# Performance work log

Hardware: AMD Instinct MI355X
Metric: run time of the kernel (lower is better)

## Reference

```python
import jax, jax.numpy as jnp
import numpy as np

N = 50000   # nodes
E = 800000  # edges (avg degree 16)
D = 128     # hidden dim (GNN_hidden_dim), heads=1
SLOPE = 0.2  # LeakyReLU negative slope (PyG default)


def _w(k, shape, fan_in):
    return jax.random.normal(k, shape, dtype=jnp.float32) * (1.0 / np.sqrt(fan_in))


def setup_inputs() -> dict:
    key = jax.random.key(0)
    ks = jax.random.split(key, 24)
    inp = {}
    inp["x"] = jax.random.normal(ks[0], (N, D), dtype=jnp.float32)
    inp["edge_index"] = jax.random.randint(ks[1], (2, E), 0, N, dtype=jnp.int32)
    # layer 1 (GATv2 + linear skip)
    inp["Wl1"] = _w(ks[2], (D, D), D); inp["Wr1"] = _w(ks[3], (D, D), D)
    inp["att1"] = _w(ks[4], (D,), D); inp["b1"] = jnp.zeros((D,), jnp.float32)
    inp["Wlin1"] = _w(ks[5], (D, D), D); inp["blin1"] = jnp.zeros((D,), jnp.float32)
    # layer 2
    inp["Wl2"] = _w(ks[6], (D, D), D); inp["Wr2"] = _w(ks[7], (D, D), D)
    inp["att2"] = _w(ks[8], (D,), D); inp["b2"] = jnp.zeros((D,), jnp.float32)
    inp["Wlin2"] = _w(ks[9], (D, D), D); inp["blin2"] = jnp.zeros((D,), jnp.float32)
    # output layer (out_channels=1, heads=1)
    inp["Wlo"] = _w(ks[10], (D, 1), D); inp["Wro"] = _w(ks[11], (D, 1), D)
    inp["atto"] = _w(ks[12], (1,), 1); inp["bo"] = jnp.zeros((1,), jnp.float32)
    inp["Wlino"] = _w(ks[13], (D, 1), D); inp["blino"] = jnp.zeros((1,), jnp.float32)
    return inp


def gatv2(x, src, dst, Wl, Wr, att, b):
    # GATv2 (PyG, add_self_loops=False, share_weights=False, heads=1, no edge_attr)
    xl = x @ Wl            # [N, C] source transform (also message content)
    xr = x @ Wr            # [N, C] target transform
    e = jax.nn.leaky_relu(xl[src] + xr[dst], SLOPE) @ att  # [E] edge logits
    m = jax.ops.segment_max(e, dst, num_segments=N)
    m = jnp.where(jnp.isfinite(m), m, 0.0)  # empty segments
    p = jnp.exp(e - m[dst])
    s = jax.ops.segment_sum(p, dst, num_segments=N)
    alpha = p / (s[dst] + 1e-16)            # segment softmax over incoming edges
    out = jax.ops.segment_sum(alpha[:, None] * xl[src], dst, num_segments=N)
    return out + b


def reference(x, edge_index, Wl1, Wr1, att1, b1, Wlin1, blin1,
              Wl2, Wr2, att2, b2, Wlin2, blin2,
              Wlo, Wro, atto, bo, Wlino, blino):
    src, dst = edge_index[0], edge_index[1]
    h = jax.nn.relu(gatv2(x, src, dst, Wl1, Wr1, att1, b1) + x @ Wlin1 + blin1)
    h = jax.nn.relu(gatv2(h, src, dst, Wl2, Wr2, att2, b2) + h @ Wlin2 + blin2)
    out = gatv2(h, src, dst, Wlo, Wro, atto, bo) + h @ Wlino + blino
    return out  # [N, 1]
```

## Files before the change

### kernel.cpp

```cpp
#include <hip/hip_runtime.h>
#include <hip/hip_fp16.h>
#include <math.h>

#define NN 50000
#define EE 800000
#define DD 128
#define SLOPE 0.2f

typedef __attribute__((ext_vector_type(8))) _Float16 half8;
typedef __attribute__((ext_vector_type(4))) float f32x4;

static __device__ __forceinline__ float wred_sum(float v) {
#pragma unroll
    for (int m = 1; m < 64; m <<= 1) v += __shfl_xor(v, m, 64);
    return v;
}

static __device__ __forceinline__ ushort f2h(float f) {
    __half h = __float2half(f);
    return *reinterpret_cast<ushort*>(&h);
}
static __device__ __forceinline__ __half2 u2h2(unsigned int u) {
    __half2 h;
    *reinterpret_cast<unsigned int*>(&h) = u;
    return h;
}
static __device__ __forceinline__ unsigned int h22u(__half2 h) {
    return *reinterpret_cast<unsigned int*>(&h);
}

__global__ void k_degree(const int* __restrict__ dstv, int* __restrict__ deg,
                         int* __restrict__ epos) {
    int i = blockIdx.x * blockDim.x + threadIdx.x;
    if (i < EE) epos[i] = atomicAdd(&deg[dstv[i]], 1);
}

__global__ void k_blocksum(const int* __restrict__ deg, int* __restrict__ bsum) {
    int t = threadIdx.x;
    int idx = blockIdx.x * 256 + t;
    int v = (idx < NN) ? deg[idx] : 0;
#pragma unroll
    for (int m = 1; m < 64; m <<= 1) v += __shfl_xor(v, m, 64);
    __shared__ int part[4];
    if ((t & 63) == 0) part[t >> 6] = v;
    __syncthreads();
    if (t == 0) bsum[blockIdx.x] = part[0] + part[1] + part[2] + part[3];
}

__global__ void k_scan_bsum(const int* __restrict__ bsum, int* __restrict__ boff, int nb) {
    __shared__ int sd[2][256];
    int t = threadIdx.x;
    int v = (t < nb) ? bsum[t] : 0;
    sd[0][t] = v;
    __syncthreads();
    int s = 0;
    for (int off = 1; off < 256; off <<= 1) {
        int x = sd[s][t];
        if (t >= off) x += sd[s][t - off];
        sd[s ^ 1][t] = x;
        s ^= 1;
        __syncthreads();
    }
    if (t < nb) boff[t] = sd[s][t] - v;
}

__global__ void k_scan_final(const int* __restrict__ deg, const int* __restrict__ boff,
                             int* __restrict__ offs) {
    __shared__ int sd[2][256];
    int t = threadIdx.x;
    int idx = blockIdx.x * 256 + t;
    int v = (idx < NN) ? deg[idx] : 0;
    sd[0][t] = v;
    __syncthreads();
    int s = 0;
    for (int off = 1; off < 256; off <<= 1) {
        int x = sd[s][t];
        if (t >= off) x += sd[s][t - off];
        sd[s ^ 1][t] = x;
        s ^= 1;
        __syncthreads();
    }
    int incl = sd[s][t];
    int base = boff[blockIdx.x];
    if (idx < NN) offs[idx + 1] = base + incl;
    if (idx == 0) offs[0] = 0;
}

__global__ void k_scatter(const int* __restrict__ srcv, const int* __restrict__ dstv,
                          const int* __restrict__ offs, const int* __restrict__ epos,
                          int* __restrict__ csr_src) {
    int i = blockIdx.x * blockDim.x + threadIdx.x;
    if (i < EE) csr_src[offs[dstv[i]] + epos[i]] = srcv[i];
}

__global__ __launch_bounds__(256) void k_wconvert(
    const float* __restrict__ W0, const float* __restrict__ W1, const float* __restrict__ W2,
    const float* __restrict__ W3, const float* __restrict__ W4, const float* __restrict__ W5,
    ushort* __restrict__ Wt) {
    int idx = blockIdx.x * 256 + threadIdx.x;
    int i = idx >> 14;
    int r = idx & 16383;
    int n = r >> 7;
    int k = r & 127;
    const float* Ws[6] = {W0, W1, W2, W3, W4, W5};
    Wt[idx] = f2h(Ws[i][k * DD + n]);
}

template <int XBF>
__global__ __launch_bounds__(256) void k_gemm3m(
    const float* __restrict__ Xf,
    const ushort* __restrict__ Xb,
    const ushort* __restrict__ Wt,
    ushort* __restrict__ O0b,
    ushort* __restrict__ O1b,
    ushort* __restrict__ O2b) {
    __shared__ ushort wsh[128 * 136];
    int t = threadIdx.x;
    int wid = t >> 6, lane = t & 63;
    int m0 = blockIdx.x * 128 + wid * 32;
    int qrow = lane & 15, kg = lane >> 4;

    half8 afrag[2][4];
#pragma unroll
    for (int mg = 0; mg < 2; mg++) {
#pragma unroll
        for (int ks = 0; ks < 4; ks++) {
            int row = m0 + mg * 16 + qrow;
            row = (row < NN) ? row : (NN - 1);
            if (XBF) {
                afrag[mg][ks] = *reinterpret_cast<const half8*>(
                    Xb + (size_t)row * DD + ks * 32 + kg * 8);
            } else {
                const float* p = Xf + (size_t)row * DD + ks * 32 + kg * 8;
                float4 u0 = *reinterpret_cast<const float4*>(p);
                float4 u1 = *reinterpret_cast<const float4*>(p + 4);
                half8 s;
                s[0] = (_Float16)u0.x; s[1] = (_Float16)u0.y;
                s[2] = (_Float16)u0.z; s[3] = (_Float16)u0.w;
                s[4] = (_Float16)u1.x; s[5] = (_Float16)u1.y;
                s[6] = (_Float16)u1.z; s[7] = (_Float16)u1.w;
                afrag[mg][ks] = s;
            }
        }
    }

    for (int w = 0; w < 3; w++) {
        __syncthreads();
        const ushort* Wb = Wt + (size_t)w * DD * DD;
#pragma unroll
        for (int i = 0; i < 8; i++) {
            int flat = i * 256 + t;
            int row = flat >> 4, ch = flat & 15;
            half8 v = *reinterpret_cast<const half8*>(Wb + row * DD + ch * 8);
            *reinterpret_cast<half8*>(&wsh[row * 136 + ch * 8]) = v;
        }
        __syncthreads();

        f32x4 acc[2][8];
#pragma unroll
        for (int mg = 0; mg < 2; mg++)
#pragma unroll
            for (int ng = 0; ng < 8; ng++) acc[mg][ng] = (f32x4)(0.f);

#pragma unroll
        for (int ks = 0; ks < 4; ks++) {
            half8 bfrag[8];
#pragma unroll
            for (int ng = 0; ng < 8; ng++)
                bfrag[ng] = *reinterpret_cast<const half8*>(
                    &wsh[(ng * 16 + qrow) * 136 + ks * 32 + kg * 8]);
#pragma unroll
            for (int mg = 0; mg < 2; mg++)
#pragma unroll
                for (int ng = 0; ng < 8; ng++)
                    acc[mg][ng] = __builtin_amdgcn_mfma_f32_16x16x32_f16(
                        afrag[mg][ks], bfrag[ng], acc[mg][ng], 0, 0, 0);
        }

        ushort* Ob = (w == 0) ? O0b : (w == 1) ? O1b : O2b;
#pragma unroll
        for (int mg = 0; mg < 2; mg++) {
#pragma unroll
            for (int r = 0; r < 4; r++) {
                int row = m0 + mg * 16 + kg * 4 + r;
                if (row < NN) {
#pragma unroll
                    for (int ng = 0; ng < 8; ng++) {
                        int col = ng * 16 + qrow;
                        Ob[(size_t)row * DD + col] = f2h(acc[mg][ng][r]);
                    }
                }
            }
        }
    }
}

template <int OUTVEC>
__global__ __launch_bounds__(64) void k_fused(
    const int* __restrict__ offs, const int* __restrict__ csr_src,
    const ushort* __restrict__ xlb,
    const ushort* __restrict__ xrb,
    const float* __restrict__ att,
    const ushort* __restrict__ linb,
    const float* __restrict__ bb,
    const float* __restrict__ blin, ushort* __restrict__ houtb,
    const float* __restrict__ Wlo, const float* __restrict__ Wro,
    const float* __restrict__ Wlino, const float* __restrict__ blino,
    float* __restrict__ xlo, float* __restrict__ xro, float* __restrict__ lino) {
    int wid = blockIdx.x;
    int lane = threadIdx.x;
    int q = lane >> 4;
    int ql = lane & 15;
    int c0 = ql * 8;

    __half2 av6h[4], av4h[4];
    {
        float4 a0 = *reinterpret_cast<const float4*>(att + c0);
        float4 a1 = *reinterpret_cast<const float4*>(att + c0 + 4);
        float av[8] = {a0.x, a0.y, a0.z, a0.w, a1.x, a1.y, a1.z, a1.w};
#pragma unroll
        for (int c = 0; c < 4; c++) {
            av6h[c] = __halves2half2(__float2half(0.6f * av[2 * c]),
                                     __float2half(0.6f * av[2 * c + 1]));
            av4h[c] = __halves2half2(__float2half(0.4f * av[2 * c]),
                                     __float2half(0.4f * av[2 * c + 1]));
        }
    }
    __half2 xrv2[4];
    {
        uint4 xrp = *reinterpret_cast<const uint4*>(xrb + (size_t)wid * DD + c0);
        xrv2[0] = u2h2(xrp.x); xrv2[1] = u2h2(xrp.y);
        xrv2[2] = u2h2(xrp.z); xrv2[3] = u2h2(xrp.w);
    }

    int start = offs[wid];
    int deg = offs[wid + 1] - start;

    float ss = 0.f;
    __half2 acc2[4];
#pragma unroll
    for (int c = 0; c < 4; c++) acc2[c] = u2h2(0u);

    for (int eb = 0; eb < deg; eb += 64) {
        int nb = min(64, deg - eb);
        int myidx = (lane < nb) ? csr_src[start + eb + lane] : 0;
        int rounds = (nb + 3) >> 2;
        for (int r = 0; r < rounds; r++) {
            int j = r * 4 + q;
            bool ok = j < nb;
            int s = __shfl(myidx, j, 64);
            uint4 xp = *reinterpret_cast<const uint4*>(xlb + (size_t)s * DD + c0);
            __half2 xv2[4] = {u2h2(xp.x), u2h2(xp.y), u2h2(xp.z), u2h2(xp.w)};
            __half2 vs = u2h2(0u);
#pragma unroll
            for (int c = 0; c < 4; c++) {
                __half2 u2 = __hadd2(xv2[c], xrv2[c]);
                __half2 a2 = u2h2(h22u(u2) & 0x7fff7fffu);
                vs = __hfma2(u2, av6h[c], vs);
                vs = __hfma2(a2, av4h[c], vs);
            }
            float v = __low2float(vs) + __high2float(vs);
#pragma unroll
            for (int msk = 1; msk < 16; msk <<= 1) v += __shfl_xor(v, msk, 64);
            float p = ok ? __expf(v) : 0.f;
            ss += p;
            __half2 p2 = __float2half2_rn(p);
#pragma unroll
            for (int c = 0; c < 4; c++) acc2[c] = __hfma2(p2, xv2[c], acc2[c]);
        }
    }

#pragma unroll
    for (int msk = 16; msk < 64; msk <<= 1) {
        ss += __shfl_xor(ss, msk, 64);
#pragma unroll
        for (int c = 0; c < 4; c++) {
            unsigned int o = (unsigned int)__shfl_xor((int)h22u(acc2[c]), msk, 64);
            acc2[c] = __hadd2(acc2[c], u2h2(o));
        }
    }

    if (q == 0) {
        float inv = 1.f / (ss + 1e-16f);
        float o[8];
#pragma unroll
        for (int c = 0; c < 4; c++) {
            o[2 * c] = __low2float(acc2[c]) * inv;
            o[2 * c + 1] = __high2float(acc2[c]) * inv;
        }
        float lv[8];
        {
            uint4 lp = *reinterpret_cast<const uint4*>(linb + (size_t)wid * DD + c0);
            __half2 l2[4] = {u2h2(lp.x), u2h2(lp.y), u2h2(lp.z), u2h2(lp.w)};
#pragma unroll
            for (int c = 0; c < 4; c++) {
                lv[2 * c] = __low2float(l2[c]);
                lv[2 * c + 1] = __high2float(l2[c]);
            }
        }
        float4 b0 = *reinterpret_cast<const float4*>(bb + c0);
        float4 b1 = *reinterpret_cast<const float4*>(bb + c0 + 4);
        float4 bl0 = *reinterpret_cast<const float4*>(blin + c0);
        float4 bl1 = *reinterpret_cast<const float4*>(blin + c0 + 4);
        float bv[8] = {b0.x, b0.y, b0.z, b0.w, b1.x, b1.y, b1.z, b1.w};
        float blv[8] = {bl0.x, bl0.y, bl0.z, bl0.w, bl1.x, bl1.y, bl1.z, bl1.w};
#pragma unroll
        for (int c = 0; c < 8; c++) o[c] = fmaxf(o[c] + bv[c] + lv[c] + blv[c], 0.f);

        if (!OUTVEC) {
            uint4 pk;
            pk.x = (unsigned)f2h(o[0]) | ((unsigned)f2h(o[1]) << 16);
            pk.y = (unsigned)f2h(o[2]) | ((unsigned)f2h(o[3]) << 16);
            pk.z = (unsigned)f2h(o[4]) | ((unsigned)f2h(o[5]) << 16);
            pk.w = (unsigned)f2h(o[6]) | ((unsigned)f2h(o[7]) << 16);
            *reinterpret_cast<uint4*>(houtb + (size_t)wid * DD + c0) = pk;
        } else {
            float4 w0a = *reinterpret_cast<const float4*>(Wlo + c0);
            float4 w0b = *reinterpret_cast<const float4*>(Wlo + c0 + 4);
            float4 w1a = *reinterpret_cast<const float4*>(Wro + c0);
            float4 w1b = *reinterpret_cast<const float4*>(Wro + c0 + 4);
            float4 w2a = *reinterpret_cast<const float4*>(Wlino + c0);
            float4 w2b = *reinterpret_cast<const float4*>(Wlino + c0 + 4);
            float wv0[8] = {w0a.x, w0a.y, w0a.z, w0a.w, w0b.x, w0b.y, w0b.z, w0b.w};
            float wv1[8] = {w1a.x, w1a.y, w1a.z, w1a.w, w1b.x, w1b.y, w1b.z, w1b.w};
            float wv2[8] = {w2a.x, w2a.y, w2a.z, w2a.w, w2b.x, w2b.y, w2b.z, w2b.w};
            float d0 = 0.f, d1 = 0.f, d2 = 0.f;
#pragma unroll
            for (int c = 0; c < 8; c++) {
                d0 += o[c] * wv0[c];
                d1 += o[c] * wv1[c];
                d2 += o[c] * wv2[c];
            }
#pragma unroll
            for (int msk = 1; msk < 16; msk <<= 1) {
                d0 += __shfl_xor(d0, msk, 64);
                d1 += __shfl_xor(d1, msk, 64);
                d2 += __shfl_xor(d2, msk, 64);
            }
            if (ql == 0) {
                xlo[wid] = d0;
                xro[wid] = d1;
                lino[wid] = d2 + blino[0];
            }
        }
    }
}

__global__ __launch_bounds__(256) void k_aggout(
    const int* __restrict__ offs, const int* __restrict__ csr_src,
    const float* __restrict__ xlo, const float* __restrict__ xro,
    const float* __restrict__ atto, const float* __restrict__ lino,
    const float* __restrict__ bo, float* __restrict__ out) {
    int wid = (blockIdx.x * blockDim.x + threadIdx.x) >> 6;
    int lane = threadIdx.x & 63;
    if (wid >= NN) return;
    int start = offs[wid];
    int deg = offs[wid + 1] - start;
    float xro_w = xro[wid];
    float a0 = atto[0];

    float sl = 0.f, nl = 0.f;
    for (int j = lane; j < deg; j += 64) {
        int s = csr_src[start + j];
        float xs = xlo[s];
        float u = xs + xro_w;
        float e = fmaxf(u, SLOPE * u) * a0;
        float p = __expf(e);
        sl += p;
        nl += p * xs;
    }
    sl = wred_sum(sl);
    nl = wred_sum(nl);
    if (lane == 0) out[wid] = nl / (sl + 1e-16f) + bo[0] + lino[wid];
}

extern "C" void kernel_launch(void* const* d_in, const int* in_sizes, int n_in,
                              void* d_out, int out_size, void* d_ws, size_t ws_size,
                              hipStream_t stream) {
    const float* x = (const float*)d_in[0];
    const int* ei = (const int*)d_in[1];
    const int* srcv = ei;
    const int* dstv = ei + EE;
    const float* Wl1 = (const float*)d_in[2];
    const float* Wr1 = (const float*)d_in[3];
    const float* att1 = (const float*)d_in[4];
    const float* b1 = (const float*)d_in[5];
    const float* Wlin1 = (const float*)d_in[6];
    const float* blin1 = (const float*)d_in[7];
    const float* Wl2 = (const float*)d_in[8];
    const float* Wr2 = (const float*)d_in[9];
    const float* att2 = (const float*)d_in[10];
    const float* b2 = (const float*)d_in[11];
    const float* Wlin2 = (const float*)d_in[12];
    const float* blin2 = (const float*)d_in[13];
    const float* Wlo = (const float*)d_in[14];
    const float* Wro = (const float*)d_in[15];
    const float* atto = (const float*)d_in[16];
    const float* bo = (const float*)d_in[17];
    const float* Wlino = (const float*)d_in[18];
    const float* blino = (const float*)d_in[19];

    char* w = (char*)d_ws;
    auto alloc = [&](size_t bytes) {
        void* p = (void*)w;
        w += (bytes + 255) & ~(size_t)255;
        return p;
    };
    ushort* xlb = (ushort*)alloc((size_t)NN * DD * 2);
    ushort* xrb = (ushort*)alloc((size_t)NN * DD * 2);
    ushort* linb = (ushort*)alloc((size_t)NN * DD * 2);
    ushort* hb = (ushort*)alloc((size_t)NN * DD * 2);
    ushort* Wt = (ushort*)alloc((size_t)6 * DD * DD * 2);
    float* xlo = (float*)alloc((size_t)NN * 4);
    float* xro = (float*)alloc((size_t)NN * 4);
    float* lino = (float*)alloc((size_t)NN * 4);
    int* deg = (int*)alloc((size_t)NN * 4);
    int* offs = (int*)alloc((size_t)(NN + 1) * 4);
    int* bsum = (int*)alloc(256 * 4);
    int* boff = (int*)alloc(256 * 4);
    int* csr_src = (int*)alloc((size_t)(EE + 64) * 4);
    int* epos = (int*)alloc((size_t)EE * 4);

    const int NB = (NN + 255) / 256;

    hipMemsetAsync(deg, 0, (size_t)NN * 4, stream);
    k_degree<<<(EE + 255) / 256, 256, 0, stream>>>(dstv, deg, epos);
    k_blocksum<<<NB, 256, 0, stream>>>(deg, bsum);
    k_scan_bsum<<<1, 256, 0, stream>>>(bsum, boff, NB);
    k_scan_final<<<NB, 256, 0, stream>>>(deg, boff, offs);
    k_scatter<<<(EE + 255) / 256, 256, 0, stream>>>(srcv, dstv, offs, epos, csr_src);

    k_wconvert<<<(6 * DD * DD) / 256, 256, 0, stream>>>(Wl1, Wr1, Wlin1, Wl2, Wr2, Wlin2, Wt);

    const int GEMM_GRID = (NN + 127) / 128;
    const int NODE_GRID = (NN * 64 + 255) / 256;

    k_gemm3m<0><<<GEMM_GRID, 256, 0, stream>>>(x, nullptr, Wt + (size_t)0 * 3 * DD * DD,
                                               xlb, xrb, linb);
    k_fused<0><<<NN, 64, 0, stream>>>(offs, csr_src, xlb, xrb, att1, linb, b1, blin1, hb,
                                      nullptr, nullptr, nullptr, nullptr,
                                      nullptr, nullptr, nullptr);
    k_gemm3m<1><<<GEMM_GRID, 256, 0, stream>>>(nullptr, hb, Wt + (size_t)1 * 3 * DD * DD,
                                               xlb, xrb, linb);
    k_fused<1><<<NN, 64, 0, stream>>>(offs, csr_src, xlb, xrb, att2, linb, b2, blin2,
                                      nullptr, Wlo, Wro, Wlino, blino,
                                      xlo, xro, lino);
    k_aggout<<<NODE_GRID, 256, 0, stream>>>(offs, csr_src, xlo, xro, atto, lino, bo, (float*)d_out);
}
```

Measured before the change: 192.1 us.

## Pack two nodes per block and unroll edge gather loop by two

```diff
diff --git a/kernel.cpp b/kernel.cpp
--- a/kernel.cpp
+++ b/kernel.cpp
@@ -196,7 +196,7 @@
 }
 
 template <int OUTVEC>
-__global__ __launch_bounds__(64) void k_fused(
+__global__ __launch_bounds__(128) void k_fused(
     const int* __restrict__ offs, const int* __restrict__ csr_src,
     const ushort* __restrict__ xlb,
     const ushort* __restrict__ xrb,
@@ -207,8 +207,9 @@
     const float* __restrict__ Wlo, const float* __restrict__ Wro,
     const float* __restrict__ Wlino, const float* __restrict__ blino,
     float* __restrict__ xlo, float* __restrict__ xro, float* __restrict__ lino) {
-    int wid = blockIdx.x;
-    int lane = threadIdx.x;
+    int wid = blockIdx.x * 2 + (threadIdx.x >> 6);
+    if (wid >= NN) return;
+    int lane = threadIdx.x & 63;
     int q = lane >> 4;
     int ql = lane & 15;
     int c0 = ql * 8;
@@ -245,7 +246,48 @@
         int nb = min(64, deg - eb);
         int myidx = (lane < nb) ? csr_src[start + eb + lane] : 0;
         int rounds = (nb + 3) >> 2;
-        for (int r = 0; r < rounds; r++) {
+        int r = 0;
+        for (; r + 2 <= rounds; r += 2) {
+            int j0 = r * 4 + q;
+            int j1 = j0 + 4;
+            bool ok1 = j1 < nb;
+            int s0 = __shfl(myidx, j0, 64);
+            int s1 = __shfl(myidx, j1, 64);
+            uint4 xp0 = *reinterpret_cast<const uint4*>(xlb + (size_t)s0 * DD + c0);
+            uint4 xp1 = *reinterpret_cast<const uint4*>(xlb + (size_t)s1 * DD + c0);
+            __half2 xa[4] = {u2h2(xp0.x), u2h2(xp0.y), u2h2(xp0.z), u2h2(xp0.w)};
+            __half2 xb[4] = {u2h2(xp1.x), u2h2(xp1.y), u2h2(xp1.z), u2h2(xp1.w)};
+            __half2 va = u2h2(0u), vb = u2h2(0u);
+#pragma unroll
+            for (int c = 0; c < 4; c++) {
+                __half2 ua = __hadd2(xa[c], xrv2[c]);
+                __half2 ub = __hadd2(xb[c], xrv2[c]);
+                __half2 aa = u2h2(h22u(ua) & 0x7fff7fffu);
+                __half2 ab = u2h2(h22u(ub) & 0x7fff7fffu);
+                va = __hfma2(ua, av6h[c], va);
+                vb = __hfma2(ub, av6h[c], vb);
+                va = __hfma2(aa, av4h[c], va);
+                vb = __hfma2(ab, av4h[c], vb);
+            }
+            float v0 = __low2float(va) + __high2float(va);
+            float v1 = __low2float(vb) + __high2float(vb);
+#pragma unroll
+            for (int msk = 1; msk < 16; msk <<= 1) {
+                v0 += __shfl_xor(v0, msk, 64);
+                v1 += __shfl_xor(v1, msk, 64);
+            }
+            float p0 = __expf(v0);
+            float p1 = ok1 ? __expf(v1) : 0.f;
+            ss += p0 + p1;
+            __half2 p20 = __float2half2_rn(p0);
+            __half2 p21 = __float2half2_rn(p1);
+#pragma unroll
+            for (int c = 0; c < 4; c++) {
+                acc2[c] = __hfma2(p20, xa[c], acc2[c]);
+                acc2[c] = __hfma2(p21, xb[c], acc2[c]);
+            }
+        }
+        if (r < rounds) {
             int j = r * 4 + q;
             bool ok = j < nb;
             int s = __shfl(myidx, j, 64);
@@ -433,17 +475,18 @@
     k_wconvert<<<(6 * DD * DD) / 256, 256, 0, stream>>>(Wl1, Wr1, Wlin1, Wl2, Wr2, Wlin2, Wt);
 
     const int GEMM_GRID = (NN + 127) / 128;
+    const int FUSED_GRID = (NN + 1) / 2;
     const int NODE_GRID = (NN * 64 + 255) / 256;
 
     k_gemm3m<0><<<GEMM_GRID, 256, 0, stream>>>(x, nullptr, Wt + (size_t)0 * 3 * DD * DD,
                                                xlb, xrb, linb);
-    k_fused<0><<<NN, 64, 0, stream>>>(offs, csr_src, xlb, xrb, att1, linb, b1, blin1, hb,
-                                      nullptr, nullptr, nullptr, nullptr,
-                                      nullptr, nullptr, nullptr);
+    k_fused<0><<<FUSED_GRID, 128, 0, stream>>>(offs, csr_src, xlb, xrb, att1, linb, b1, blin1, hb,
+                                               nullptr, nullptr, nullptr, nullptr,
+                                               nullptr, nullptr, nullptr);
     k_gemm3m<1><<<GEMM_GRID, 256, 0, stream>>>(nullptr, hb, Wt + (size_t)1 * 3 * DD * DD,
                                                xlb, xrb, linb);
-    k_fused<1><<<NN, 64, 0, stream>>>(offs, csr_src, xlb, xrb, att2, linb, b2, blin2,
-                                      nullptr, Wlo, Wro, Wlino, blino,
-                                      xlo, xro, lino);
+    k_fused<1><<<FUSED_GRID, 128, 0, stream>>>(offs, csr_src, xlb, xrb, att2, linb, b2, blin2,
+                                               nullptr, Wlo, Wro, Wlino, blino,
+                                               xlo, xro, lino);
     k_aggout<<<NODE_GRID, 256, 0, stream>>>(offs, csr_src, xlo, xro, atto, lino, bo, (float*)d_out);
 }
```

After: 189.8 us. No clear change (-1.2%).
